# Performance work log

Measured on AMD Instinct MI355X. Metric: run time of the kernel, lower is better.

The kernel has to match this reference:

```python
import jax, jax.numpy as jnp
import numpy as np

B, T, D, H, L = 8, 512, 768, 12, 12
OBS, VOCAB, MAXT, BLK = 128, 6, 4096, 1023
S = 2 * T          # interleaved state/action token sequence
DH = D // H
DFF = 4 * D


def _ln(x, g, b):
    m = jnp.mean(x, -1, keepdims=True)
    v = jnp.mean((x - m) ** 2, -1, keepdims=True)
    return (x - m) * jax.lax.rsqrt(v + 1e-5) * g + b


def setup_inputs() -> dict:
    key = jax.random.key(0)
    ks = jax.random.split(key, 24)
    p = lambda k, shape: (jax.random.normal(k, shape, jnp.float32) * 0.02)
    return {
        'states': jax.random.normal(ks[0], (B, T, OBS), jnp.float32),
        'actions': jax.random.randint(ks[1], (B, T, 1), 0, VOCAB),
        'timesteps': jax.random.randint(ks[2], (B, 1, 1), 0, MAXT + 1),
        'W_s': p(ks[3], (OBS, D)), 'b_s': jnp.zeros((D,), jnp.float32),
        'A_emb': p(ks[4], (VOCAB, D)),
        'pos_emb': p(ks[5], (1, BLK + 1, D)),
        'gpos_emb': p(ks[6], (1, MAXT + 1, D)),
        'ln1_g': jnp.ones((L, D), jnp.float32), 'ln1_b': jnp.zeros((L, D), jnp.float32),
        'Wq': p(ks[7], (L, D, D)), 'bq': jnp.zeros((L, D), jnp.float32),
        'Wk': p(ks[8], (L, D, D)), 'bk': jnp.zeros((L, D), jnp.float32),
        'Wv': p(ks[9], (L, D, D)), 'bv': jnp.zeros((L, D), jnp.float32),
        'Wp': p(ks[10], (L, D, D)), 'bp': jnp.zeros((L, D), jnp.float32),
        'ln2_g': jnp.ones((L, D), jnp.float32), 'ln2_b': jnp.zeros((L, D), jnp.float32),
        'W1': p(ks[11], (L, D, DFF)), 'b1': jnp.zeros((L, DFF), jnp.float32),
        'W2': p(ks[12], (L, DFF, D)), 'b2': jnp.zeros((L, D), jnp.float32),
        'lnf_g': jnp.ones((D,), jnp.float32), 'lnf_b': jnp.zeros((D,), jnp.float32),
    }


def reference(states, actions, timesteps, W_s, b_s, A_emb, pos_emb, gpos_emb,
              ln1_g, ln1_b, Wq, bq, Wk, bk, Wv, bv, Wp, bp,
              ln2_g, ln2_b, W1, b1, W2, b2, lnf_g, lnf_b):
    # encoders
    se = jnp.tanh(states @ W_s + b_s)                       # [B,T,D]
    ae = jnp.tanh(A_emb[actions[..., 0]])                   # [B,T,D]
    # interleave: s0,a0,s1,a1,... -> [B,S,D]
    tok = jnp.stack([se, ae], axis=2).reshape(B, S, D)
    # global positional (one timestep gathered per batch) + local positional
    gpos = gpos_emb[0][timesteps[:, 0, 0]][:, None, :]      # [B,1,D]
    x = tok + gpos + pos_emb[:, :S, :]
    mask = jnp.tril(jnp.ones((S, S), dtype=bool))
    scale = 1.0 / np.sqrt(DH).astype(np.float32)
    for l in range(L):
        h = _ln(x, ln1_g[l], ln1_b[l])
        q = (h @ Wq[l] + bq[l]).reshape(B, S, H, DH)
        k = (h @ Wk[l] + bk[l]).reshape(B, S, H, DH)
        v = (h @ Wv[l] + bv[l]).reshape(B, S, H, DH)
        att = jnp.einsum('bqhd,bkhd->bhqk', q, k) * scale
        att = jnp.where(mask[None, None], att, -jnp.inf)
        att = jax.nn.softmax(att, axis=-1)
        y = jnp.einsum('bhqk,bkhd->bqhd', att, v).reshape(B, S, D)
        x = x + y @ Wp[l] + bp[l]
        h = _ln(x, ln2_g[l], ln2_b[l])
        x = x + jax.nn.gelu(h @ W1[l] + b1[l], approximate=False) @ W2[l] + b2[l]
    x = _ln(x, lnf_g, lnf_b)
    return x[:, ::2, :]                                     # state_output [B,T,D]
```

## Files before the change

kernel.cpp:

```cpp
#include <hip/hip_runtime.h>
#include <hip/hip_bf16.h>

#define B_   8
#define T_   512
#define S_   1024
#define D_   768
#define H_   12
#define DH_  64
#define L_   12
#define DFF_ 3072
#define M_   8192
#define QKVD 2304

typedef float f32x4 __attribute__((ext_vector_type(4)));
typedef short b16x8 __attribute__((ext_vector_type(8)));

#define LDS_CAST(p) ((__attribute__((address_space(3))) void*)(unsigned)(unsigned long long)(p))
#define GBL_CAST(p) ((const __attribute__((address_space(1))) void*)(unsigned long long)(p))

__device__ inline short f2b(float f) {
  unsigned u = __builtin_bit_cast(unsigned, f);
  unsigned r = u + 0x7fffu + ((u >> 16) & 1u);
  return (short)(unsigned short)(r >> 16);
}
__device__ inline float b2f(short s) {
  unsigned u = ((unsigned)(unsigned short)s) << 16;
  return __builtin_bit_cast(float, u);
}
__device__ inline float gelu_f(float v) {
  const float e = __expf(v * (1.5957691216f + 0.0713548162f * v * v));
  return v * e / (e + 1.0f);
}
__device__ inline float tanh_f(float v) {
  const float e = __expf(2.0f * v);
  return 1.0f - 2.0f / (e + 1.0f);
}

__global__ __launch_bounds__(256) void cvt_kernel(const float* __restrict__ in,
                                                  short* __restrict__ out, int n) {
  const int i = (blockIdx.x * 256 + threadIdx.x) * 4;
  if (i < n) {
    const f32x4 v = *(const f32x4*)&in[i];
    out[i] = f2b(v.x); out[i + 1] = f2b(v.y); out[i + 2] = f2b(v.z); out[i + 3] = f2b(v.w);
  }
}

__global__ __launch_bounds__(256) void trconv_kernel(const float* __restrict__ W,
                                                     short* __restrict__ Wt,
                                                     int K, int N) {
  __shared__ float tile[32][33];
  const int k0 = blockIdx.x * 32, n0 = blockIdx.y * 32;
  const int tx = threadIdx.x & 31, ty = threadIdx.x >> 5;
  #pragma unroll
  for (int i = ty; i < 32; i += 8) tile[i][tx] = W[(size_t)(k0 + i) * N + (n0 + tx)];
  __syncthreads();
  #pragma unroll
  for (int i = ty; i < 32; i += 8) Wt[(size_t)(n0 + i) * K + (k0 + tx)] = f2b(tile[tx][i]);
}

__global__ __launch_bounds__(256) void trconv_layer(const float* __restrict__ Wq,
                                                    const float* __restrict__ Wk,
                                                    const float* __restrict__ Wv,
                                                    const float* __restrict__ Wp,
                                                    const float* __restrict__ W1,
                                                    const float* __restrict__ W2,
                                                    short* __restrict__ Dqkv,
                                                    short* __restrict__ Dp,
                                                    short* __restrict__ D1,
                                                    short* __restrict__ D2) {
  __shared__ float tile[32][33];
  int id = blockIdx.x;
  const float* W; short* Dst; int K, N, kt, nt;
  if (id < 2304) {
    const int wsel = id / 576; id -= wsel * 576;
    W   = (wsel == 0) ? Wq : (wsel == 1) ? Wk : (wsel == 2) ? Wv : Wp;
    Dst = (wsel == 3) ? Dp : (Dqkv + (size_t)wsel * D_ * D_);
    K = D_; N = D_; kt = id / 24; nt = id % 24;
  } else if (id < 4608) {
    id -= 2304; W = W1; Dst = D1; K = D_; N = DFF_; kt = id / 96; nt = id % 96;
  } else {
    id -= 4608; W = W2; Dst = D2; K = DFF_; N = D_; kt = id / 24; nt = id % 24;
  }
  const int k0 = kt * 32, n0 = nt * 32;
  const int tx = threadIdx.x & 31, ty = threadIdx.x >> 5;
  #pragma unroll
  for (int i = ty; i < 32; i += 8) tile[i][tx] = W[(size_t)(k0 + i) * N + (n0 + tx)];
  __syncthreads();
  #pragma unroll
  for (int i = ty; i < 32; i += 8) Dst[(size_t)(n0 + i) * K + (k0 + tx)] = f2b(tile[tx][i]);
}

__global__ __launch_bounds__(256) void embed2_kernel(
    const short* __restrict__ se, const int* __restrict__ actions,
    const int* __restrict__ timesteps, const float* __restrict__ A_emb,
    const float* __restrict__ pos_emb, const float* __restrict__ gpos_emb,
    float* __restrict__ x) {
  const int bt = blockIdx.x;
  const int b = bt >> 9, t = bt & 511;
  const int tid = threadIdx.x;
  const int act = actions[bt];
  const int ts = timesteps[b];
  const float* gp = gpos_emb + (size_t)ts * D_;
  #pragma unroll
  for (int i = 0; i < 3; ++i) {
    const int d = tid + i * 256;
    const float sev = b2f(se[(size_t)bt * D_ + d]);
    const float aev = tanhf(A_emb[act * D_ + d]);
    const float g = gp[d];
    const size_t base = ((size_t)b * S_ + 2 * t) * D_ + d;
    x[base]      = sev + g + pos_emb[(2 * t) * D_ + d];
    x[base + D_] = aev + g + pos_emb[(2 * t + 1) * D_ + d];
  }
}

__global__ __launch_bounds__(256) void ln_kernel(const float* __restrict__ x,
                                                 const float* __restrict__ gg,
                                                 const float* __restrict__ bb,
                                                 short* __restrict__ out) {
  __shared__ float red[4];
  const int row = blockIdx.x, tid = threadIdx.x;
  const float* xr = x + (size_t)row * D_;
  float v0 = xr[tid], v1 = xr[tid + 256], v2 = xr[tid + 512];
  float s = v0 + v1 + v2;
  #pragma unroll
  for (int o = 32; o > 0; o >>= 1) s += __shfl_xor(s, o);
  if ((tid & 63) == 0) red[tid >> 6] = s;
  __syncthreads();
  const float mean = (red[0] + red[1] + red[2] + red[3]) * (1.0f / D_);
  __syncthreads();
  const float d0 = v0 - mean, d1 = v1 - mean, d2 = v2 - mean;
  float s2 = d0 * d0 + d1 * d1 + d2 * d2;
  #pragma unroll
  for (int o = 32; o > 0; o >>= 1) s2 += __shfl_xor(s2, o);
  if ((tid & 63) == 0) red[tid >> 6] = s2;
  __syncthreads();
  const float inv = rsqrtf((red[0] + red[1] + red[2] + red[3]) * (1.0f / D_) + 1e-5f);
  short* orow = out + (size_t)row * D_;
  orow[tid]       = f2b(d0 * inv * gg[tid] + bb[tid]);
  orow[tid + 256] = f2b(d1 * inv * gg[tid + 256] + bb[tid + 256]);
  orow[tid + 512] = f2b(d2 * inv * gg[tid + 512] + bb[tid + 512]);
}

template <int MODE>
__global__ __launch_bounds__(256) void reduce2_kernel(
    const float* __restrict__ P, const float* __restrict__ bias,
    float* __restrict__ x, const float* __restrict__ gg,
    const float* __restrict__ bb, short* __restrict__ h,
    float* __restrict__ out) {
  __shared__ float red[4];
  const int row = blockIdx.x, tid = threadIdx.x;
  if (MODE == 2 && (row & 1)) return;
  const float* p0 = P + (size_t)row * D_;
  const float* p1 = P + (size_t)M_ * D_ + (size_t)row * D_;
  float* xr = x + (size_t)row * D_;
  float v0 = xr[tid]       + p0[tid]       + p1[tid]       + bias[tid];
  float v1 = xr[tid + 256] + p0[tid + 256] + p1[tid + 256] + bias[tid + 256];
  float v2 = xr[tid + 512] + p0[tid + 512] + p1[tid + 512] + bias[tid + 512];
  if (MODE == 1) { xr[tid] = v0; xr[tid + 256] = v1; xr[tid + 512] = v2; }
  float s = v0 + v1 + v2;
  #pragma unroll
  for (int o = 32; o > 0; o >>= 1) s += __shfl_xor(s, o);
  if ((tid & 63) == 0) red[tid >> 6] = s;
  __syncthreads();
  const float mean = (red[0] + red[1] + red[2] + red[3]) * (1.0f / D_);
  __syncthreads();
  const float d0 = v0 - mean, d1 = v1 - mean, d2 = v2 - mean;
  float s2 = d0 * d0 + d1 * d1 + d2 * d2;
  #pragma unroll
  for (int o = 32; o > 0; o >>= 1) s2 += __shfl_xor(s2, o);
  if ((tid & 63) == 0) red[tid >> 6] = s2;
  __syncthreads();
  const float inv = rsqrtf((red[0] + red[1] + red[2] + red[3]) * (1.0f / D_) + 1e-5f);
  if (MODE == 1) {
    short* orow = h + (size_t)row * D_;
    orow[tid]       = f2b(d0 * inv * gg[tid] + bb[tid]);
    orow[tid + 256] = f2b(d1 * inv * gg[tid + 256] + bb[tid + 256]);
    orow[tid + 512] = f2b(d2 * inv * gg[tid + 512] + bb[tid + 512]);
  } else {
    const int b = row >> 10, t = (row & 1023) >> 1;
    float* orow = out + ((size_t)b * T_ + t) * D_;
    orow[tid]       = d0 * inv * gg[tid] + bb[tid];
    orow[tid + 256] = d1 * inv * gg[tid + 256] + bb[tid + 256];
    orow[tid + 512] = d2 * inv * gg[tid + 512] + bb[tid + 512];
  }
}

__device__ __forceinline__ void mainloop128(const short* __restrict__ gA,
                                            const short* __restrict__ gB,
                                            int K, int kIters,
                                            short* As, short* Bs,
                                            int wave, int l15, int lq, int wr, int wc,
                                            f32x4 (&acc)[4][4]) {
  auto STAGE = [&](int kt, int buf) {
    const short* a = gA + kt * 32;
    const short* b = gB + kt * 32;
    short* la = As + buf * 4096 + wave * 512;
    short* lb = Bs + buf * 4096 + wave * 512;
    __builtin_amdgcn_global_load_lds(GBL_CAST(a),                  LDS_CAST(la),        16, 0, 0);
    __builtin_amdgcn_global_load_lds(GBL_CAST(a + (size_t)64 * K), LDS_CAST(la + 2048), 16, 0, 0);
    __builtin_amdgcn_global_load_lds(GBL_CAST(b),                  LDS_CAST(lb),        16, 0, 0);
    __builtin_amdgcn_global_load_lds(GBL_CAST(b + (size_t)64 * K), LDS_CAST(lb + 2048), 16, 0, 0);
  };
  STAGE(0, 0);
  asm volatile("s_waitcnt vmcnt(0)" ::: "memory");
  __builtin_amdgcn_s_barrier();
  __builtin_amdgcn_sched_barrier(0);
  int cur = 0;
  for (int kt = 0; kt < kIters; ++kt) {
    if (kt + 1 < kIters) STAGE(kt + 1, cur ^ 1);
    const short* Ab = As + cur * 4096;
    const short* Bb = Bs + cur * 4096;
    b16x8 af[4], bfr[4];
    #pragma unroll
    for (int i = 0; i < 4; ++i)
      af[i] = *(const b16x8*)&Ab[(wr * 64 + i * 16 + l15) * 32 + lq * 8];
    #pragma unroll
    for (int j = 0; j < 4; ++j)
      bfr[j] = *(const b16x8*)&Bb[(wc * 64 + j * 16 + l15) * 32 + lq * 8];
    __builtin_amdgcn_s_setprio(1);
    #pragma unroll
    for (int i = 0; i < 4; ++i)
      #pragma unroll
      for (int j = 0; j < 4; ++j)
        acc[i][j] = __builtin_amdgcn_mfma_f32_16x16x32_bf16(af[i], bfr[j], acc[i][j], 0, 0, 0);
    __builtin_amdgcn_s_setprio(0);
    asm volatile("s_waitcnt vmcnt(0)" ::: "memory");
    __builtin_amdgcn_s_barrier();
    __builtin_amdgcn_sched_barrier(0);
    cur ^= 1;
  }
}

template <int EPI>
__global__ __launch_bounds__(256) void gemm_bf16(const short* __restrict__ A,
                                                 const short* __restrict__ Bt,
                                                 const float* __restrict__ bias,
                                                 short* __restrict__ Cb,
                                                 int M, int N, int K) {
  __shared__ __align__(16) short As[8192];
  __shared__ __align__(16) short Bs[8192];
  const int tid = threadIdx.x;
  const int wave = tid >> 6, lane = tid & 63;
  const int l15 = lane & 15, lq = lane >> 4;
  const int wr = wave >> 1, wc = wave & 1;
  const int row0 = blockIdx.x * 128, col0 = blockIdx.y * 128;

  const short* gA = A + (size_t)(row0 + (tid >> 2)) * K + (tid & 3) * 8;
  const short* gB = Bt + (size_t)(col0 + (tid >> 2)) * K + (tid & 3) * 8;
  f32x4 acc[4][4] = {};
  mainloop128(gA, gB, K, K / 32, As, Bs, wave, l15, lq, wr, wc, acc);

  #pragma unroll
  for (int i = 0; i < 4; ++i) {
    #pragma unroll
    for (int j = 0; j < 4; ++j) {
      const int col = col0 + wc * 64 + j * 16 + l15;
      const float bv = bias[col];
      #pragma unroll
      for (int r = 0; r < 4; ++r) {
        const int row = row0 + wr * 64 + i * 16 + lq * 4 + r;
        const float v = acc[i][j][r] + bv;
        const size_t idx = (size_t)row * N + col;
        if (EPI == 1) Cb[idx] = f2b(gelu_f(v));
        else          Cb[idx] = f2b(tanh_f(v));
      }
    }
  }
}

__global__ __launch_bounds__(256) void gemm_splitk(const short* __restrict__ A,
                                                   const short* __restrict__ Bt,
                                                   float* __restrict__ P,
                                                   int M, int N, int K, int KC) {
  __shared__ __align__(16) short As[8192];
  __shared__ __align__(16) short Bs[8192];
  const int tid = threadIdx.x;
  const int wave = tid >> 6, lane = tid & 63;
  const int l15 = lane & 15, lq = lane >> 4;
  const int wr = wave >> 1, wc = wave & 1;
  const int row0 = blockIdx.x * 128, col0 = blockIdx.y * 128;
  const int k0 = blockIdx.z * KC;

  const short* gA = A + (size_t)(row0 + (tid >> 2)) * K + (tid & 3) * 8 + k0;
  const short* gB = Bt + (size_t)(col0 + (tid >> 2)) * K + (tid & 3) * 8 + k0;
  f32x4 acc[4][4] = {};
  mainloop128(gA, gB, K, KC / 32, As, Bs, wave, l15, lq, wr, wc, acc);

  float* Pz = P + (size_t)blockIdx.z * M * N;
  #pragma unroll
  for (int i = 0; i < 4; ++i) {
    #pragma unroll
    for (int j = 0; j < 4; ++j) {
      const int col = col0 + wc * 64 + j * 16 + l15;
      #pragma unroll
      for (int r = 0; r < 4; ++r) {
        const int row = row0 + wr * 64 + i * 16 + lq * 4 + r;
        Pz[(size_t)row * N + col] = acc[i][j][r];
      }
    }
  }
}

__global__ __launch_bounds__(256) void gemm_qkv(const short* __restrict__ A,
                                                const short* __restrict__ Bt,
                                                const float* __restrict__ bq,
                                                const float* __restrict__ bk,
                                                const float* __restrict__ bv,
                                                short* __restrict__ Cb, int K) {
  __shared__ __align__(16) short As[8192];
  __shared__ __align__(16) short Bs[8192];
  const int tid = threadIdx.x;
  const int wave = tid >> 6, lane = tid & 63;
  const int l15 = lane & 15, lq = lane >> 4;
  const int wr = wave >> 1, wc = wave & 1;
  const int row0 = blockIdx.x * 128, col0 = blockIdx.y * 128;
  const int seg = col0 / D_;
  const float* bias = (seg == 0) ? bq : (seg == 1) ? bk : bv;
  const float scale = (seg == 0) ? 0.125f : 1.0f;

  const short* gA = A + (size_t)(row0 + (tid >> 2)) * K + (tid & 3) * 8;
  const short* gB = Bt + (size_t)(col0 + (tid >> 2)) * K + (tid & 3) * 8;
  f32x4 acc[4][4] = {};
  mainloop128(gA, gB, K, K / 32, As, Bs, wave, l15, lq, wr, wc, acc);

  #pragma unroll
  for (int i = 0; i < 4; ++i) {
    #pragma unroll
    for (int j = 0; j < 4; ++j) {
      const int col = col0 + wc * 64 + j * 16 + l15;
      const float bv = bias[col - seg * D_];
      #pragma unroll
      for (int r = 0; r < 4; ++r) {
        const int row = row0 + wr * 64 + i * 16 + lq * 4 + r;
        Cb[(size_t)row * QKVD + col] = f2b((acc[i][j][r] + bv) * scale);
      }
    }
  }
}

__global__ __launch_bounds__(256) void gemm64(const short* __restrict__ A,
                                              const short* __restrict__ Bt,
                                              const float* __restrict__ bias,
                                              float* __restrict__ Xres,
                                              int M, int N, int K) {
  __shared__ __align__(16) short As[4096];
  __shared__ __align__(16) short Bs[8192];
  const int tid = threadIdx.x;
  const int wave = tid >> 6, lane = tid & 63;
  const int l15 = lane & 15, lq = lane >> 4;
  const int wr = wave >> 1, wc = wave & 1;
  const int row0 = blockIdx.x * 64, col0 = blockIdx.y * 128;

  const short* gA = A + (size_t)(row0 + (tid >> 2)) * K + (tid & 3) * 8;
  const short* gB = Bt + (size_t)(col0 + (tid >> 2)) * K + (tid & 3) * 8;

  auto STAGE = [&](int kt, int buf) {
    const short* a = gA + kt * 32;
    const short* b = gB + kt * 32;
    short* la = As + buf * 2048 + wave * 512;
    short* lb = Bs + buf * 4096 + wave * 512;
    __builtin_amdgcn_global_load_lds(GBL_CAST(a),                  LDS_CAST(la),        16, 0, 0);
    __builtin_amdgcn_global_load_lds(GBL_CAST(b),                  LDS_CAST(lb),        16, 0, 0);
    __builtin_amdgcn_global_load_lds(GBL_CAST(b + (size_t)64 * K), LDS_CAST(lb + 2048), 16, 0, 0);
  };

  f32x4 acc[2][4] = {};
  STAGE(0, 0);
  asm volatile("s_waitcnt vmcnt(0)" ::: "memory");
  __builtin_amdgcn_s_barrier();
  __builtin_amdgcn_sched_barrier(0);
  int cur = 0;
  const int kIters = K / 32;
  for (int kt = 0; kt < kIters; ++kt) {
    if (kt + 1 < kIters) STAGE(kt + 1, cur ^ 1);
    const short* Ab = As + cur * 2048;
    const short* Bb = Bs + cur * 4096;
    b16x8 af[2], bfr[4];
    #pragma unroll
    for (int i = 0; i < 2; ++i)
      af[i] = *(const b16x8*)&Ab[(wr * 32 + i * 16 + l15) * 32 + lq * 8];
    #pragma unroll
    for (int j = 0; j < 4; ++j)
      bfr[j] = *(const b16x8*)&Bb[(wc * 64 + j * 16 + l15) * 32 + lq * 8];
    __builtin_amdgcn_s_setprio(1);
    #pragma unroll
    for (int i = 0; i < 2; ++i)
      #pragma unroll
      for (int j = 0; j < 4; ++j)
        acc[i][j] = __builtin_amdgcn_mfma_f32_16x16x32_bf16(af[i], bfr[j], acc[i][j], 0, 0, 0);
    __builtin_amdgcn_s_setprio(0);
    asm volatile("s_waitcnt vmcnt(0)" ::: "memory");
    __builtin_amdgcn_s_barrier();
    __builtin_amdgcn_sched_barrier(0);
    cur ^= 1;
  }
  #pragma unroll
  for (int i = 0; i < 2; ++i) {
    #pragma unroll
    for (int j = 0; j < 4; ++j) {
      const int col = col0 + wc * 64 + j * 16 + l15;
      const float bv = bias[col];
      #pragma unroll
      for (int r = 0; r < 4; ++r) {
        const int row = row0 + wr * 32 + i * 16 + lq * 4 + r;
        Xres[(size_t)row * N + col] += acc[i][j][r] + bv;
      }
    }
  }
}

__global__ __launch_bounds__(256) void attn_kernel(const short* __restrict__ qkv,
                                                   short* __restrict__ yb) {
  __shared__ __align__(16) short Ks[2][4096];
  __shared__ __align__(16) short Vt[2][64 * 72];
  __shared__ __align__(16) short Ps[4][16 * 88];

  const int bh = blockIdx.x, pair = blockIdx.y;
  const int h = bh % H_, b = bh / H_;
  const int tid = threadIdx.x, wave = tid >> 6, lane = tid & 63;
  const int l15 = lane & 15, lq = lane >> 4;

  const int r0 = tid >> 3, c0 = tid & 7;
  const int r1 = (tid + 256) >> 3;
  const int vkey = tid >> 2, vdhg = tid & 3;

  for (int t2 = 0; t2 < 2; ++t2) {
    const int qt = t2 ? (15 - pair) : pair;
    const int nkt = qt + 1;
    const int qrow0 = qt * 64 + wave * 16;

    const short* qp = qkv + (size_t)(b * S_ + qrow0 + l15) * QKVD + h * 64 + lq * 8;
    const b16x8 qf0 = *(const b16x8*)qp;
    const b16x8 qf1 = *(const b16x8*)(qp + 32);

    f32x4 o[4] = {};
    float lacc[4] = {0.f, 0.f, 0.f, 0.f};

    auto stage = [&](int kt, int s) {
      const int kbase = kt * 64;
      const short* gk0 = qkv + (size_t)(b * S_ + kbase + r0) * QKVD + D_ + h * 64 + ((c0 ^ (r0 & 7)) * 8);
      __builtin_amdgcn_global_load_lds(GBL_CAST(gk0), LDS_CAST(&Ks[s][wave * 512]), 16, 0, 0);
      const short* gk1 = qkv + (size_t)(b * S_ + kbase + r1) * QKVD + D_ + h * 64 + ((c0 ^ (r1 & 7)) * 8);
      __builtin_amdgcn_global_load_lds(GBL_CAST(gk1), LDS_CAST(&Ks[s][2048 + wave * 512]), 16, 0, 0);
      const short* gv = qkv + (size_t)(b * S_ + kbase + vkey) * QKVD + 2 * D_ + h * 64 + vdhg * 16;
      const b16x8 v0 = *(const b16x8*)gv;
      const b16x8 v1 = *(const b16x8*)(gv + 8);
      #pragma unroll
      for (int e = 0; e < 8; ++e) Vt[s][(vdhg * 16 + e) * 72 + vkey] = v0[e];
      #pragma unroll
      for (int e = 0; e < 8; ++e) Vt[s][(vdhg * 16 + 8 + e) * 72 + vkey] = v1[e];
    };

    stage(0, 0);
    __syncthreads();

    for (int kt = 0; kt < nkt; ++kt) {
      const int cur = kt & 1;
      if (kt + 1 < nkt) stage(kt + 1, cur ^ 1);
      const int kbase = kt * 64;
      const bool needmask = (kt == qt);

      f32x4 s4[4];
      #pragma unroll
      for (int j = 0; j < 4; ++j) {
        const int krow = j * 16 + l15;
        const b16x8 kf0 = *(const b16x8*)&Ks[cur][krow * 64 + ((lq ^ (krow & 7)) * 8)];
        const b16x8 kf1 = *(const b16x8*)&Ks[cur][krow * 64 + (((4 + lq) ^ (krow & 7)) * 8)];
        f32x4 z = {};
        z = __builtin_amdgcn_mfma_f32_16x16x32_bf16(qf0, kf0, z, 0, 0, 0);
        s4[j] = __builtin_amdgcn_mfma_f32_16x16x32_bf16(qf1, kf1, z, 0, 0, 0);
      }

      #pragma unroll
      for (int r = 0; r < 4; ++r) {
        const int q = qrow0 + lq * 4 + r;
        float psum = 0.f;
        #pragma unroll
        for (int j = 0; j < 4; ++j) {
          float pp = __expf(s4[j][r]);
          if (needmask && (kbase + j * 16 + l15 > q)) pp = 0.f;
          psum += pp;
          Ps[wave][(lq * 4 + r) * 88 + j * 16 + l15] = f2b(pp);
        }
        lacc[r] += psum;
      }

      #pragma unroll
      for (int c = 0; c < 2; ++c) {
        const b16x8 pf = *(const b16x8*)&Ps[wave][l15 * 88 + c * 32 + lq * 8];
        #pragma unroll
        for (int jn = 0; jn < 4; ++jn) {
          const b16x8 vf = *(const b16x8*)&Vt[cur][(jn * 16 + l15) * 72 + c * 32 + lq * 8];
          o[jn] = __builtin_amdgcn_mfma_f32_16x16x32_bf16(pf, vf, o[jn], 0, 0, 0);
        }
      }
      __syncthreads();
    }

    #pragma unroll
    for (int r = 0; r < 4; ++r) {
      #pragma unroll
      for (int ofs = 1; ofs < 16; ofs <<= 1) lacc[r] += __shfl_xor(lacc[r], ofs);
      lacc[r] = 1.0f / lacc[r];
    }

    #pragma unroll
    for (int jn = 0; jn < 4; ++jn) {
      #pragma unroll
      for (int r = 0; r < 4; ++r) {
        const int q = qrow0 + lq * 4 + r;
        const int dh = jn * 16 + l15;
        yb[(size_t)(b * S_ + q) * D_ + h * 64 + dh] = f2b(o[jn][r] * lacc[r]);
      }
    }
  }
}

extern "C" void kernel_launch(void* const* d_in, const int* in_sizes, int n_in,
                              void* d_out, int out_size, void* d_ws, size_t ws_size,
                              hipStream_t stream) {
  (void)in_sizes; (void)n_in; (void)out_size; (void)ws_size;
  const float* states    = (const float*)d_in[0];
  const int*   actions   = (const int*)d_in[1];
  const int*   timesteps = (const int*)d_in[2];
  const float* W_s       = (const float*)d_in[3];
  const float* b_s       = (const float*)d_in[4];
  const float* A_emb     = (const float*)d_in[5];
  const float* pos_emb   = (const float*)d_in[6];
  const float* gpos_emb  = (const float*)d_in[7];
  const float* ln1_g     = (const float*)d_in[8];
  const float* ln1_b     = (const float*)d_in[9];
  const float* Wq        = (const float*)d_in[10];
  const float* bq        = (const float*)d_in[11];
  const float* Wk        = (const float*)d_in[12];
  const float* bk        = (const float*)d_in[13];
  const float* Wv        = (const float*)d_in[14];
  const float* bv        = (const float*)d_in[15];
  const float* Wp        = (const float*)d_in[16];
  const float* bp        = (const float*)d_in[17];
  const float* ln2_g     = (const float*)d_in[18];
  const float* ln2_b     = (const float*)d_in[19];
  const float* W1        = (const float*)d_in[20];
  const float* b1        = (const float*)d_in[21];
  const float* W2        = (const float*)d_in[22];
  const float* b2        = (const float*)d_in[23];
  const float* lnf_g     = (const float*)d_in[24];
  const float* lnf_b     = (const float*)d_in[25];
  float* out = (float*)d_out;

  char* p = (char*)d_ws;
  float* x    = (float*)p; p += (size_t)M_ * D_ * 4;
  short* h    = (short*)p; p += (size_t)M_ * D_ * 2;
  short* qkv  = (short*)p; p += (size_t)M_ * QKVD * 2;
  short* y    = (short*)p; p += (size_t)M_ * D_ * 2;
  short* gbf  = (short*)p; p += (size_t)M_ * DFF_ * 2;
  short* wqkvt= (short*)p; p += (size_t)QKVD * D_ * 2;
  short* wpt  = (short*)p; p += (size_t)D_ * D_ * 2;
  short* w1t  = (short*)p; p += (size_t)D_ * DFF_ * 2;
  short* w2t  = (short*)p; p += (size_t)D_ * DFF_ * 2;
  float* Pbuf = (float*)qkv;
  short* sbf  = qkv;
  short* wst  = qkv + (size_t)4096 * 128;
  short* se   = gbf;

  cvt_kernel<<<(B_ * T_ * 128) / 1024, 256, 0, stream>>>(states, sbf, B_ * T_ * 128);
  trconv_kernel<<<dim3(4, 24), 256, 0, stream>>>(W_s, wst, 128, D_);
  gemm_bf16<4><<<dim3(32, 6), 256, 0, stream>>>(sbf, wst, b_s, se, 4096, D_, 128);
  embed2_kernel<<<B_ * T_, 256, 0, stream>>>(se, actions, timesteps, A_emb, pos_emb, gpos_emb, x);
  ln_kernel<<<M_, 256, 0, stream>>>(x, ln1_g, ln1_b, h);

  for (int l = 0; l < L_; ++l) {
    trconv_layer<<<6912, 256, 0, stream>>>(
        Wq + (size_t)l * D_ * D_, Wk + (size_t)l * D_ * D_,
        Wv + (size_t)l * D_ * D_, Wp + (size_t)l * D_ * D_,
        W1 + (size_t)l * D_ * DFF_, W2 + (size_t)l * D_ * DFF_,
        wqkvt, wpt, w1t, w2t);

    gemm_qkv<<<dim3(M_ / 128, QKVD / 128), 256, 0, stream>>>(h, wqkvt, bq + l * D_, bk + l * D_, bv + l * D_, qkv, D_);
    attn_kernel<<<dim3(B_ * H_, 8), 256, 0, stream>>>(qkv, y);
    gemm64<<<dim3(M_ / 64, D_ / 128), 256, 0, stream>>>(y, wpt, bp + l * D_, x, M_, D_, D_);
    ln_kernel<<<M_, 256, 0, stream>>>(x, ln2_g + l * D_, ln2_b + l * D_, h);
    gemm_bf16<1><<<dim3(M_ / 128, DFF_ / 128), 256, 0, stream>>>(h, w1t, b1 + l * DFF_, gbf, M_, DFF_, D_);
    gemm_splitk<<<dim3(M_ / 128, D_ / 128, 2), 256, 0, stream>>>(gbf, w2t, Pbuf, M_, D_, DFF_, DFF_ / 2);
    if (l < L_ - 1) {
      reduce2_kernel<1><<<M_, 256, 0, stream>>>(Pbuf, b2 + l * D_, x,
                                                ln1_g + (l + 1) * D_, ln1_b + (l + 1) * D_, h, nullptr);
    } else {
      reduce2_kernel<2><<<M_, 256, 0, stream>>>(Pbuf, b2 + l * D_, x, lnf_g, lnf_b, nullptr, out);
    }
  }
}
```

Baseline: 3.035 ms.

## Triple-buffer GEMM mainloops with partial waitcnt and XOR-swizzled LDS layout

```diff
diff --git a/kernel.cpp b/kernel.cpp
--- a/kernel.cpp
+++ b/kernel.cpp
@@ -202,21 +202,27 @@
     __builtin_amdgcn_global_load_lds(GBL_CAST(b + (size_t)64 * K), LDS_CAST(lb + 2048), 16, 0, 0);
   };
   STAGE(0, 0);
-  asm volatile("s_waitcnt vmcnt(0)" ::: "memory");
-  __builtin_amdgcn_s_barrier();
-  __builtin_amdgcn_sched_barrier(0);
-  int cur = 0;
+  if (kIters > 1) STAGE(1, 1);
+  const int coff = (lq ^ ((l15 >> 1) & 3)) * 8;
+  int b0 = 0, b1 = 1, b2 = 2;
   for (int kt = 0; kt < kIters; ++kt) {
-    if (kt + 1 < kIters) STAGE(kt + 1, cur ^ 1);
-    const short* Ab = As + cur * 4096;
-    const short* Bb = Bs + cur * 4096;
+    if (kt + 1 < kIters) {
+      asm volatile("s_waitcnt vmcnt(4)" ::: "memory");
+    } else {
+      asm volatile("s_waitcnt vmcnt(0)" ::: "memory");
+    }
+    __builtin_amdgcn_s_barrier();
+    __builtin_amdgcn_sched_barrier(0);
+    if (kt + 2 < kIters) STAGE(kt + 2, b2);
+    const short* Ab = As + b0 * 4096;
+    const short* Bb = Bs + b0 * 4096;
     b16x8 af[4], bfr[4];
     #pragma unroll
     for (int i = 0; i < 4; ++i)
-      af[i] = *(const b16x8*)&Ab[(wr * 64 + i * 16 + l15) * 32 + lq * 8];
+      af[i] = *(const b16x8*)&Ab[(wr * 64 + i * 16 + l15) * 32 + coff];
     #pragma unroll
     for (int j = 0; j < 4; ++j)
-      bfr[j] = *(const b16x8*)&Bb[(wc * 64 + j * 16 + l15) * 32 + lq * 8];
+      bfr[j] = *(const b16x8*)&Bb[(wc * 64 + j * 16 + l15) * 32 + coff];
     __builtin_amdgcn_s_setprio(1);
     #pragma unroll
     for (int i = 0; i < 4; ++i)
@@ -224,10 +230,7 @@
       for (int j = 0; j < 4; ++j)
         acc[i][j] = __builtin_amdgcn_mfma_f32_16x16x32_bf16(af[i], bfr[j], acc[i][j], 0, 0, 0);
     __builtin_amdgcn_s_setprio(0);
-    asm volatile("s_waitcnt vmcnt(0)" ::: "memory");
-    __builtin_amdgcn_s_barrier();
-    __builtin_amdgcn_sched_barrier(0);
-    cur ^= 1;
+    const int t = b0; b0 = b1; b1 = b2; b2 = t;
   }
 }
 
@@ -237,16 +240,17 @@
                                                  const float* __restrict__ bias,
                                                  short* __restrict__ Cb,
                                                  int M, int N, int K) {
-  __shared__ __align__(16) short As[8192];
-  __shared__ __align__(16) short Bs[8192];
+  __shared__ __align__(16) short As[12288];
+  __shared__ __align__(16) short Bs[12288];
   const int tid = threadIdx.x;
   const int wave = tid >> 6, lane = tid & 63;
   const int l15 = lane & 15, lq = lane >> 4;
   const int wr = wave >> 1, wc = wave & 1;
   const int row0 = blockIdx.x * 128, col0 = blockIdx.y * 128;
-
-  const short* gA = A + (size_t)(row0 + (tid >> 2)) * K + (tid & 3) * 8;
-  const short* gB = Bt + (size_t)(col0 + (tid >> 2)) * K + (tid & 3) * 8;
+  const int acs = ((tid & 3) ^ ((tid >> 3) & 3)) * 8;
+
+  const short* gA = A + (size_t)(row0 + (tid >> 2)) * K + acs;
+  const short* gB = Bt + (size_t)(col0 + (tid >> 2)) * K + acs;
   f32x4 acc[4][4] = {};
   mainloop128(gA, gB, K, K / 32, As, Bs, wave, l15, lq, wr, wc, acc);
 
@@ -272,17 +276,18 @@
                                                    const short* __restrict__ Bt,
                                                    float* __restrict__ P,
                                                    int M, int N, int K, int KC) {
-  __shared__ __align__(16) short As[8192];
-  __shared__ __align__(16) short Bs[8192];
+  __shared__ __align__(16) short As[12288];
+  __shared__ __align__(16) short Bs[12288];
   const int tid = threadIdx.x;
   const int wave = tid >> 6, lane = tid & 63;
   const int l15 = lane & 15, lq = lane >> 4;
   const int wr = wave >> 1, wc = wave & 1;
   const int row0 = blockIdx.x * 128, col0 = blockIdx.y * 128;
   const int k0 = blockIdx.z * KC;
-
-  const short* gA = A + (size_t)(row0 + (tid >> 2)) * K + (tid & 3) * 8 + k0;
-  const short* gB = Bt + (size_t)(col0 + (tid >> 2)) * K + (tid & 3) * 8 + k0;
+  const int acs = ((tid & 3) ^ ((tid >> 3) & 3)) * 8;
+
+  const short* gA = A + (size_t)(row0 + (tid >> 2)) * K + acs + k0;
+  const short* gB = Bt + (size_t)(col0 + (tid >> 2)) * K + acs + k0;
   f32x4 acc[4][4] = {};
   mainloop128(gA, gB, K, KC / 32, As, Bs, wave, l15, lq, wr, wc, acc);
 
@@ -307,8 +312,8 @@
                                                 const float* __restrict__ bk,
                                                 const float* __restrict__ bv,
                                                 short* __restrict__ Cb, int K) {
-  __shared__ __align__(16) short As[8192];
-  __shared__ __align__(16) short Bs[8192];
+  __shared__ __align__(16) short As[12288];
+  __shared__ __align__(16) short Bs[12288];
   const int tid = threadIdx.x;
   const int wave = tid >> 6, lane = tid & 63;
   const int l15 = lane & 15, lq = lane >> 4;
@@ -317,9 +322,10 @@
   const int seg = col0 / D_;
   const float* bias = (seg == 0) ? bq : (seg == 1) ? bk : bv;
   const float scale = (seg == 0) ? 0.125f : 1.0f;
-
-  const short* gA = A + (size_t)(row0 + (tid >> 2)) * K + (tid & 3) * 8;
-  const short* gB = Bt + (size_t)(col0 + (tid >> 2)) * K + (tid & 3) * 8;
+  const int acs = ((tid & 3) ^ ((tid >> 3) & 3)) * 8;
+
+  const short* gA = A + (size_t)(row0 + (tid >> 2)) * K + acs;
+  const short* gB = Bt + (size_t)(col0 + (tid >> 2)) * K + acs;
   f32x4 acc[4][4] = {};
   mainloop128(gA, gB, K, K / 32, As, Bs, wave, l15, lq, wr, wc, acc);
 
@@ -343,16 +349,17 @@
                                               const float* __restrict__ bias,
                                               float* __restrict__ Xres,
                                               int M, int N, int K) {
-  __shared__ __align__(16) short As[4096];
-  __shared__ __align__(16) short Bs[8192];
+  __shared__ __align__(16) short As[6144];
+  __shared__ __align__(16) short Bs[12288];
   const int tid = threadIdx.x;
   const int wave = tid >> 6, lane = tid & 63;
   const int l15 = lane & 15, lq = lane >> 4;
   const int wr = wave >> 1, wc = wave & 1;
   const int row0 = blockIdx.x * 64, col0 = blockIdx.y * 128;
-
-  const short* gA = A + (size_t)(row0 + (tid >> 2)) * K + (tid & 3) * 8;
-  const short* gB = Bt + (size_t)(col0 + (tid >> 2)) * K + (tid & 3) * 8;
+  const int acs = ((tid & 3) ^ ((tid >> 3) & 3)) * 8;
+
+  const short* gA = A + (size_t)(row0 + (tid >> 2)) * K + acs;
+  const short* gB = Bt + (size_t)(col0 + (tid >> 2)) * K + acs;
 
   auto STAGE = [&](int kt, int buf) {
     const short* a = gA + kt * 32;
@@ -365,23 +372,29 @@
   };
 
   f32x4 acc[2][4] = {};
+  const int kIters = K / 32;
   STAGE(0, 0);
-  asm volatile("s_waitcnt vmcnt(0)" ::: "memory");
-  __builtin_amdgcn_s_barrier();
-  __builtin_amdgcn_sched_barrier(0);
-  int cur = 0;
-  const int kIters = K / 32;
+  if (kIters > 1) STAGE(1, 1);
+  const int coff = (lq ^ ((l15 >> 1) & 3)) * 8;
+  int b0 = 0, b1 = 1, b2 = 2;
   for (int kt = 0; kt < kIters; ++kt) {
-    if (kt + 1 < kIters) STAGE(kt + 1, cur ^ 1);
-    const short* Ab = As + cur * 2048;
-    const short* Bb = Bs + cur * 4096;
+    if (kt + 1 < kIters) {
+      asm volatile("s_waitcnt vmcnt(3)" ::: "memory");
+    } else {
+      asm volatile("s_waitcnt vmcnt(0)" ::: "memory");
+    }
+    __builtin_amdgcn_s_barrier();
+    __builtin_amdgcn_sched_barrier(0);
+    if (kt + 2 < kIters) STAGE(kt + 2, b2);
+    const short* Ab = As + b0 * 2048;
+    const short* Bb = Bs + b0 * 4096;
     b16x8 af[2], bfr[4];
     #pragma unroll
     for (int i = 0; i < 2; ++i)
-      af[i] = *(const b16x8*)&Ab[(wr * 32 + i * 16 + l15) * 32 + lq * 8];
+      af[i] = *(const b16x8*)&Ab[(wr * 32 + i * 16 + l15) * 32 + coff];
     #pragma unroll
     for (int j = 0; j < 4; ++j)
-      bfr[j] = *(const b16x8*)&Bb[(wc * 64 + j * 16 + l15) * 32 + lq * 8];
+      bfr[j] = *(const b16x8*)&Bb[(wc * 64 + j * 16 + l15) * 32 + coff];
     __builtin_amdgcn_s_setprio(1);
     #pragma unroll
     for (int i = 0; i < 2; ++i)
@@ -389,10 +402,7 @@
       for (int j = 0; j < 4; ++j)
         acc[i][j] = __builtin_amdgcn_mfma_f32_16x16x32_bf16(af[i], bfr[j], acc[i][j], 0, 0, 0);
     __builtin_amdgcn_s_setprio(0);
-    asm volatile("s_waitcnt vmcnt(0)" ::: "memory");
-    __builtin_amdgcn_s_barrier();
-    __builtin_amdgcn_sched_barrier(0);
-    cur ^= 1;
+    const int t = b0; b0 = b1; b1 = b2; b2 = t;
   }
   #pragma unroll
   for (int i = 0; i < 2; ++i) {
```

After: 3.040 ms. Within noise of the previous version (+0.2%).
